# Performance work log

Measured on AMD Instinct MI355X. Metric: run time of the kernel, lower is better.

Reference implementation:

```python
import jax, jax.numpy as jnp
import numpy as np

D_MODEL = 1024
MLP_DIM = 4096
N_EXPERTS = 8
B, T = 4, 1024


def setup_inputs() -> dict:
    key = jax.random.key(0)
    ks = jax.random.split(key, 7)
    scale_in = (1.0 / D_MODEL) ** 0.5
    scale_out = (1.0 / MLP_DIM) ** 0.5
    # router (PyTorch Linear default init approximated with uniform kaiming-like bound)
    bound_g = (1.0 / D_MODEL) ** 0.5
    w_gate = jax.random.uniform(ks[0], (D_MODEL, N_EXPERTS), minval=-bound_g, maxval=bound_g, dtype=jnp.float32)
    b_gate = jax.random.uniform(ks[1], (N_EXPERTS,), minval=-bound_g, maxval=bound_g, dtype=jnp.float32)
    # expert weights per module's _init_weights: uniform(+-scale), zero biases
    W1 = jax.random.uniform(ks[2], (N_EXPERTS, D_MODEL, MLP_DIM), minval=-scale_in, maxval=scale_in, dtype=jnp.float32)
    b1 = jnp.zeros((N_EXPERTS, MLP_DIM), dtype=jnp.float32)
    W2 = jax.random.uniform(ks[3], (N_EXPERTS, MLP_DIM, D_MODEL), minval=-scale_out, maxval=scale_out, dtype=jnp.float32)
    b2 = jnp.zeros((N_EXPERTS, D_MODEL), dtype=jnp.float32)
    x = jax.random.normal(ks[4], (B, T, D_MODEL), dtype=jnp.float32)
    return {"x": x, "w_gate": w_gate, "b_gate": b_gate, "W1": W1, "b1": b1, "W2": W2, "b2": b2}


def reference(x, w_gate, b_gate, W1, b1, W2, b2):
    b, t, d = x.shape
    x_flat = x.reshape(b * t, d)                       # (N, d)
    # --- SwitchGate: top-1 routing (eval mode, no noise) ---
    logits = x_flat @ w_gate + b_gate                  # (N, E)
    probs = jax.nn.softmax(logits, axis=-1)
    route_p = jnp.max(probs, axis=-1)                  # (N,)
    route_idx = jnp.argmax(probs, axis=-1)             # (N,)
    # --- dense dispatch: run every expert on all tokens, select per-token ---
    h = jnp.einsum('nd,edm->enm', x_flat, W1) + b1[:, None, :]   # (E, N, mlp)
    h = jax.nn.relu(h)
    y = jnp.einsum('enm,emd->end', h, W2) + b2[:, None, :]       # (E, N, d)
    n = b * t
    out = y[route_idx, jnp.arange(n)] * route_p[:, None]         # (N, d)
    return out.reshape(b, t, d)
```

## Files before the change

### kernel.cpp

```cpp
#include <hip/hip_runtime.h>
#include <hip/hip_bf16.h>


#define D_MODEL 1024
#define MLP_DIM 4096
#define N_EXPERTS 8
#define N_TOK 4096
#define KSPLIT 4

__global__ __launch_bounds__(64) void router_kernel(
    const float* __restrict__ x, const float* __restrict__ w_gate,
    const float* __restrict__ b_gate, int* __restrict__ route_idx,
    float* __restrict__ route_p) {
  int t = blockIdx.x;
  int lane = threadIdx.x;
  const float* xr = x + (size_t)t * D_MODEL;
  float acc[N_EXPERTS];
#pragma unroll
  for (int e = 0; e < N_EXPERTS; ++e) acc[e] = 0.f;
#pragma unroll
  for (int i = 0; i < D_MODEL / 64; ++i) {
    int idx = i * 64 + lane;
    float xv = xr[idx];
    const float* wg = w_gate + (size_t)idx * N_EXPERTS;
#pragma unroll
    for (int e = 0; e < N_EXPERTS; ++e) acc[e] += xv * wg[e];
  }
#pragma unroll
  for (int off = 32; off >= 1; off >>= 1) {
#pragma unroll
    for (int e = 0; e < N_EXPERTS; ++e) acc[e] += __shfl_xor(acc[e], off, 64);
  }
  if (lane == 0) {
    float l[N_EXPERTS];
#pragma unroll
    for (int e = 0; e < N_EXPERTS; ++e) l[e] = acc[e] + b_gate[e];
    float m = l[0];
    int bi = 0;
#pragma unroll
    for (int e = 1; e < N_EXPERTS; ++e) {
      if (l[e] > m) { m = l[e]; bi = e; }
    }
    float s = 0.f;
#pragma unroll
    for (int e = 0; e < N_EXPERTS; ++e) s += expf(l[e] - m);
    route_idx[t] = bi;
    route_p[t] = 1.0f / s;
  }
}

__global__ void bucket_kernel(const int* __restrict__ route_idx,
                              int* __restrict__ counts,
                              int* __restrict__ bucket) {
  int t = blockIdx.x * blockDim.x + threadIdx.x;
  if (t < N_TOK) {
    int e = route_idx[t];
    int pos = atomicAdd(&counts[e], 1);
    bucket[e * N_TOK + pos] = t;
  }
}

template <bool SPLIT>
__global__ __launch_bounds__(256) void expert_gemm(
    const float* __restrict__ A, const float* __restrict__ B,
    const float* __restrict__ bias, float* __restrict__ C0,
    float* __restrict__ partials, const int* __restrict__ bucket,
    const int* __restrict__ counts, int Kstride, int Ncols) {
  constexpr int BM = 128, BN = 128, BK = 16;
  constexpr int LDA = BM + 4, LDB = BN + 4;
  int e, kbeg, kend;
  float* Cp;
  if (SPLIT) {
    e = blockIdx.y >> 2;
    int s = blockIdx.y & 3;
    kbeg = s * (MLP_DIM / KSPLIT);
    kend = kbeg + (MLP_DIM / KSPLIT);
    Cp = (s == 0) ? C0 : partials + (size_t)(s - 1) * N_TOK * D_MODEL;
  } else {
    e = blockIdx.y;
    kbeg = 0;
    kend = Kstride;
    Cp = C0;
  }
  int cnt = counts[e];
  int row0 = blockIdx.z * BM;
  if (row0 >= cnt) return;
  int col0 = blockIdx.x * BN;

  __shared__ float As[BK][LDA];
  __shared__ float Bs[BK][LDB];
  __shared__ int tokS[BM];

  int tid = threadIdx.x;
  if (tid < BM) {
    int r = row0 + tid;
    tokS[tid] = (r < cnt) ? bucket[e * N_TOK + r] : -1;
  }
  __syncthreads();

  const int ar = tid >> 2;
  const int ak = (tid & 3) * 4;
  const int bk = tid >> 4;
  const int bj = (tid & 15) * 8;

  const int tx = tid & 15;
  const int ty = tid >> 4;

  float acc[2][2][4][4];
#pragma unroll
  for (int hm = 0; hm < 2; ++hm)
#pragma unroll
    for (int hn = 0; hn < 2; ++hn)
#pragma unroll
      for (int i = 0; i < 4; ++i)
#pragma unroll
        for (int j = 0; j < 4; ++j) acc[hm][hn][i][j] = 0.f;

  const int tok0 = tokS[ar], tok1 = tokS[ar + 64];
  const float* __restrict__ Ap0 =
      (tok0 >= 0) ? A + (size_t)tok0 * Kstride + ak : nullptr;
  const float* __restrict__ Ap1 =
      (tok1 >= 0) ? A + (size_t)tok1 * Kstride + ak : nullptr;
  const float* __restrict__ Bp =
      B + (size_t)e * Kstride * Ncols + (size_t)bk * Ncols + col0 + bj;

  float4 a0, a1, b0, b1;
  a0 = make_float4(0.f, 0.f, 0.f, 0.f);
  a1 = a0;
  if (Ap0) a0 = *(const float4*)(Ap0 + kbeg);
  if (Ap1) a1 = *(const float4*)(Ap1 + kbeg);
  {
    const float* bp = Bp + (size_t)kbeg * Ncols;
    b0 = *(const float4*)bp;
    b1 = *(const float4*)(bp + 4);
  }

  for (int k0 = kbeg; k0 < kend; k0 += BK) {
    __syncthreads();
    As[ak + 0][ar] = a0.x; As[ak + 1][ar] = a0.y;
    As[ak + 2][ar] = a0.z; As[ak + 3][ar] = a0.w;
    As[ak + 0][ar + 64] = a1.x; As[ak + 1][ar + 64] = a1.y;
    As[ak + 2][ar + 64] = a1.z; As[ak + 3][ar + 64] = a1.w;
    *(float4*)&Bs[bk][bj] = b0;
    *(float4*)&Bs[bk][bj + 4] = b1;
    __syncthreads();

    if (k0 + BK < kend) {
      int kn = k0 + BK;
      a0 = make_float4(0.f, 0.f, 0.f, 0.f);
      a1 = a0;
      if (Ap0) a0 = *(const float4*)(Ap0 + kn);
      if (Ap1) a1 = *(const float4*)(Ap1 + kn);
      const float* bp = Bp + (size_t)kn * Ncols;
      b0 = *(const float4*)bp;
      b1 = *(const float4*)(bp + 4);
    }

#pragma unroll
    for (int kk = 0; kk < BK; ++kk) {
      float av[2][4], bv[2][4];
      *(float4*)&av[0][0] = *(const float4*)&As[kk][ty * 4];
      *(float4*)&av[1][0] = *(const float4*)&As[kk][ty * 4 + 64];
      *(float4*)&bv[0][0] = *(const float4*)&Bs[kk][tx * 4];
      *(float4*)&bv[1][0] = *(const float4*)&Bs[kk][tx * 4 + 64];
#pragma unroll
      for (int hm = 0; hm < 2; ++hm)
#pragma unroll
        for (int hn = 0; hn < 2; ++hn)
#pragma unroll
          for (int i = 0; i < 4; ++i)
#pragma unroll
            for (int j = 0; j < 4; ++j)
              acc[hm][hn][i][j] += av[hm][i] * bv[hn][j];
    }
  }

  if (SPLIT) {
#pragma unroll
    for (int hm = 0; hm < 2; ++hm) {
#pragma unroll
      for (int i = 0; i < 4; ++i) {
        int r = hm * 64 + ty * 4 + i;
        if (row0 + r < cnt) {
          int tok = tokS[r];
#pragma unroll
          for (int hn = 0; hn < 2; ++hn) {
            float4 o;
            o.x = acc[hm][hn][i][0]; o.y = acc[hm][hn][i][1];
            o.z = acc[hm][hn][i][2]; o.w = acc[hm][hn][i][3];
            *(float4*)(Cp + (size_t)tok * Ncols + col0 + hn * 64 + tx * 4) = o;
          }
        }
      }
    }
  } else {
    float4 bvv[2];
    bvv[0] = *(const float4*)(bias + (size_t)e * Ncols + col0 + tx * 4);
    bvv[1] = *(const float4*)(bias + (size_t)e * Ncols + col0 + tx * 4 + 64);
#pragma unroll
    for (int hm = 0; hm < 2; ++hm) {
#pragma unroll
      for (int i = 0; i < 4; ++i) {
        int r = hm * 64 + ty * 4 + i;
        if (row0 + r < cnt) {
          int tok = tokS[r];
#pragma unroll
          for (int hn = 0; hn < 2; ++hn) {
            const float* bb = (const float*)&bvv[hn];
            float4 o;
            o.x = fmaxf(acc[hm][hn][i][0] + bb[0], 0.f);
            o.y = fmaxf(acc[hm][hn][i][1] + bb[1], 0.f);
            o.z = fmaxf(acc[hm][hn][i][2] + bb[2], 0.f);
            o.w = fmaxf(acc[hm][hn][i][3] + bb[3], 0.f);
            *(float4*)(Cp + (size_t)tok * Ncols + col0 + hn * 64 + tx * 4) = o;
          }
        }
      }
    }
  }
}

__global__ __launch_bounds__(256) void moe_reduce_kernel(
    float* __restrict__ out, const float* __restrict__ partials,
    const float* __restrict__ b2, const int* __restrict__ route_idx,
    const float* __restrict__ route_p) {
  int tok = blockIdx.x;
  int c = threadIdx.x * 4;
  int e = route_idx[tok];
  float p = route_p[tok];
  size_t off = (size_t)tok * D_MODEL + c;
  float4 s = *(const float4*)(out + off);
  const size_t stride = (size_t)N_TOK * D_MODEL;
#pragma unroll
  for (int sp = 0; sp < KSPLIT - 1; ++sp) {
    float4 v = *(const float4*)(partials + sp * stride + off);
    s.x += v.x; s.y += v.y; s.z += v.z; s.w += v.w;
  }
  float4 bv = *(const float4*)(b2 + (size_t)e * D_MODEL + c);
  s.x = (s.x + bv.x) * p;
  s.y = (s.y + bv.y) * p;
  s.z = (s.z + bv.z) * p;
  s.w = (s.w + bv.w) * p;
  *(float4*)(out + off) = s;
}

extern "C" void kernel_launch(void* const* d_in, const int* in_sizes, int n_in,
                              void* d_out, int out_size, void* d_ws,
                              size_t ws_size, hipStream_t stream) {
  const float* x = (const float*)d_in[0];
  const float* w_gate = (const float*)d_in[1];
  const float* b_gate = (const float*)d_in[2];
  const float* W1 = (const float*)d_in[3];
  const float* b1 = (const float*)d_in[4];
  const float* W2 = (const float*)d_in[5];
  const float* b2 = (const float*)d_in[6];
  float* out = (float*)d_out;

  char* ws = (char*)d_ws;
  int* route_idx = (int*)ws;
  float* route_p = (float*)(ws + 16384);
  int* counts = (int*)(ws + 32768);
  int* bucket = (int*)(ws + 33024);
  float* H = (float*)(ws + 164096);
  float* partials = (float*)(ws + 164096 + (size_t)67108864);

  hipMemsetAsync(counts, 0, N_EXPERTS * sizeof(int), stream);
  router_kernel<<<N_TOK, 64, 0, stream>>>(x, w_gate, b_gate, route_idx, route_p);
  bucket_kernel<<<N_TOK / 256, 256, 0, stream>>>(route_idx, counts, bucket);
  expert_gemm<false><<<dim3(MLP_DIM / 128, N_EXPERTS, N_TOK / 128), 256, 0,
                       stream>>>(x, W1, b1, H, nullptr, bucket, counts,
                                 D_MODEL, MLP_DIM);
  expert_gemm<true><<<dim3(D_MODEL / 128, N_EXPERTS * KSPLIT, N_TOK / 128), 256,
                      0, stream>>>(H, W2, nullptr, out, partials, bucket,
                                   counts, MLP_DIM, D_MODEL);
  moe_reduce_kernel<<<N_TOK, 256, 0, stream>>>(out, partials, b2, route_idx,
                                               route_p);
}
```

Before: 1.268 ms.

## Schedule expert GEMMs from compact tile worklist and double-buffer shared memory

Adds a single-thread worklist kernel that lists only the non-empty (expert, row-block) tiles. Both expert GEMMs now launch a flat grid of 1280 blocks that index into that list with an XCD-aware interleaved mapping, instead of a 3D grid where most blocks exit early. The shared-memory A/B tiles are double-buffered so each iteration needs one barrier instead of two. The costs are an extra tiny serial kernel launch and twice the shared memory per block, and the grid caps the worklist at 40 tiles, which holds for 4096 tokens over 8 experts.

```diff
diff --git a/kernel.cpp b/kernel.cpp
--- a/kernel.cpp
+++ b/kernel.cpp
@@ -7,6 +7,9 @@
 #define N_EXPERTS 8
 #define N_TOK 4096
 #define KSPLIT 4
+#define WLMAX 40
+#define NWG 1280
+#define CHUNK (NWG / 8)
 
 __global__ __launch_bounds__(64) void router_kernel(
     const float* __restrict__ x, const float* __restrict__ w_gate,
@@ -60,38 +63,64 @@
   }
 }
 
+__global__ void worklist_kernel(const int* __restrict__ counts,
+                                int* __restrict__ mlist_e,
+                                int* __restrict__ mlist_r,
+                                int* __restrict__ Mp) {
+  if (threadIdx.x == 0) {
+    int m = 0;
+    for (int e = 0; e < N_EXPERTS; ++e) {
+      int c = counts[e];
+      for (int r = 0; r < c; r += 128) {
+        mlist_e[m] = e;
+        mlist_r[m] = r;
+        ++m;
+      }
+    }
+    *Mp = m;
+  }
+}
+
 template <bool SPLIT>
 __global__ __launch_bounds__(256) void expert_gemm(
     const float* __restrict__ A, const float* __restrict__ B,
     const float* __restrict__ bias, float* __restrict__ C0,
     float* __restrict__ partials, const int* __restrict__ bucket,
-    const int* __restrict__ counts, int Kstride, int Ncols) {
+    const int* __restrict__ counts, const int* __restrict__ mlist_e,
+    const int* __restrict__ mlist_r, const int* __restrict__ Mp,
+    int Kstride, int Ncols) {
   constexpr int BM = 128, BN = 128, BK = 16;
   constexpr int LDA = BM + 4, LDB = BN + 4;
-  int e, kbeg, kend;
+  const int L = blockIdx.x;
+  const int w = (L & 7) * CHUNK + (L >> 3);
+  int m, colblk, kbeg, kend;
   float* Cp;
   if (SPLIT) {
-    e = blockIdx.y >> 2;
-    int s = blockIdx.y & 3;
+    m = w % WLMAX;
+    int cs = w / WLMAX;
+    colblk = cs & 7;
+    int s = cs >> 3;
     kbeg = s * (MLP_DIM / KSPLIT);
     kend = kbeg + (MLP_DIM / KSPLIT);
     Cp = (s == 0) ? C0 : partials + (size_t)(s - 1) * N_TOK * D_MODEL;
   } else {
-    e = blockIdx.y;
+    m = w % WLMAX;
+    colblk = w / WLMAX;
     kbeg = 0;
     kend = Kstride;
     Cp = C0;
   }
-  int cnt = counts[e];
-  int row0 = blockIdx.z * BM;
-  if (row0 >= cnt) return;
-  int col0 = blockIdx.x * BN;
-
-  __shared__ float As[BK][LDA];
-  __shared__ float Bs[BK][LDB];
+  if (m >= *Mp) return;
+  const int e = mlist_e[m];
+  const int row0 = mlist_r[m];
+  const int cnt = counts[e];
+  const int col0 = colblk * BN;
+
+  __shared__ float As[2][BK][LDA];
+  __shared__ float Bs[2][BK][LDB];
   __shared__ int tokS[BM];
 
-  int tid = threadIdx.x;
+  const int tid = threadIdx.x;
   if (tid < BM) {
     int r = row0 + tid;
     tokS[tid] = (r < cnt) ? bucket[e * N_TOK + r] : -1;
@@ -125,44 +154,50 @@
       B + (size_t)e * Kstride * Ncols + (size_t)bk * Ncols + col0 + bj;
 
   float4 a0, a1, b0, b1;
-  a0 = make_float4(0.f, 0.f, 0.f, 0.f);
-  a1 = a0;
-  if (Ap0) a0 = *(const float4*)(Ap0 + kbeg);
-  if (Ap1) a1 = *(const float4*)(Ap1 + kbeg);
-  {
-    const float* bp = Bp + (size_t)kbeg * Ncols;
-    b0 = *(const float4*)bp;
-    b1 = *(const float4*)(bp + 4);
-  }
-
-  for (int k0 = kbeg; k0 < kend; k0 += BK) {
-    __syncthreads();
-    As[ak + 0][ar] = a0.x; As[ak + 1][ar] = a0.y;
-    As[ak + 2][ar] = a0.z; As[ak + 3][ar] = a0.w;
-    As[ak + 0][ar + 64] = a1.x; As[ak + 1][ar + 64] = a1.y;
-    As[ak + 2][ar + 64] = a1.z; As[ak + 3][ar + 64] = a1.w;
-    *(float4*)&Bs[bk][bj] = b0;
-    *(float4*)&Bs[bk][bj + 4] = b1;
-    __syncthreads();
-
-    if (k0 + BK < kend) {
-      int kn = k0 + BK;
-      a0 = make_float4(0.f, 0.f, 0.f, 0.f);
-      a1 = a0;
-      if (Ap0) a0 = *(const float4*)(Ap0 + kn);
-      if (Ap1) a1 = *(const float4*)(Ap1 + kn);
-      const float* bp = Bp + (size_t)kn * Ncols;
-      b0 = *(const float4*)bp;
-      b1 = *(const float4*)(bp + 4);
+
+#define LOADTILE(K0)                                          \
+  a0 = make_float4(0.f, 0.f, 0.f, 0.f);                       \
+  a1 = a0;                                                    \
+  if (Ap0) a0 = *(const float4*)(Ap0 + (K0));                 \
+  if (Ap1) a1 = *(const float4*)(Ap1 + (K0));                 \
+  {                                                           \
+    const float* bp = Bp + (size_t)(K0) * Ncols;              \
+    b0 = *(const float4*)bp;                                  \
+    b1 = *(const float4*)(bp + 4);                            \
+  }
+
+#define WRITETILE(BUF)                                        \
+  As[BUF][ak + 0][ar] = a0.x;                                 \
+  As[BUF][ak + 1][ar] = a0.y;                                 \
+  As[BUF][ak + 2][ar] = a0.z;                                 \
+  As[BUF][ak + 3][ar] = a0.w;                                 \
+  As[BUF][ak + 0][ar + 64] = a1.x;                            \
+  As[BUF][ak + 1][ar + 64] = a1.y;                            \
+  As[BUF][ak + 2][ar + 64] = a1.z;                            \
+  As[BUF][ak + 3][ar + 64] = a1.w;                            \
+  *(float4*)&Bs[BUF][bk][bj] = b0;                            \
+  *(float4*)&Bs[BUF][bk][bj + 4] = b1;
+
+  LOADTILE(kbeg);
+  WRITETILE(0);
+  __syncthreads();
+
+  const int nt = (kend - kbeg) / BK;
+  for (int t = 0; t < nt; ++t) {
+    const int cur = t & 1;
+    const bool more = (t + 1 < nt);
+    if (more) {
+      const int kn = kbeg + (t + 1) * BK;
+      LOADTILE(kn);
     }
 
 #pragma unroll
     for (int kk = 0; kk < BK; ++kk) {
       float av[2][4], bv[2][4];
-      *(float4*)&av[0][0] = *(const float4*)&As[kk][ty * 4];
-      *(float4*)&av[1][0] = *(const float4*)&As[kk][ty * 4 + 64];
-      *(float4*)&bv[0][0] = *(const float4*)&Bs[kk][tx * 4];
-      *(float4*)&bv[1][0] = *(const float4*)&Bs[kk][tx * 4 + 64];
+      *(float4*)&av[0][0] = *(const float4*)&As[cur][kk][ty * 4];
+      *(float4*)&av[1][0] = *(const float4*)&As[cur][kk][ty * 4 + 64];
+      *(float4*)&bv[0][0] = *(const float4*)&Bs[cur][kk][tx * 4];
+      *(float4*)&bv[1][0] = *(const float4*)&Bs[cur][kk][tx * 4 + 64];
 #pragma unroll
       for (int hm = 0; hm < 2; ++hm)
 #pragma unroll
@@ -173,7 +208,15 @@
             for (int j = 0; j < 4; ++j)
               acc[hm][hn][i][j] += av[hm][i] * bv[hn][j];
     }
-  }
+
+    if (more) {
+      WRITETILE(cur ^ 1);
+      __syncthreads();
+    }
+  }
+
+#undef LOADTILE
+#undef WRITETILE
 
   if (SPLIT) {
 #pragma unroll
@@ -186,8 +229,10 @@
 #pragma unroll
           for (int hn = 0; hn < 2; ++hn) {
             float4 o;
-            o.x = acc[hm][hn][i][0]; o.y = acc[hm][hn][i][1];
-            o.z = acc[hm][hn][i][2]; o.w = acc[hm][hn][i][3];
+            o.x = acc[hm][hn][i][0];
+            o.y = acc[hm][hn][i][1];
+            o.z = acc[hm][hn][i][2];
+            o.w = acc[hm][hn][i][3];
             *(float4*)(Cp + (size_t)tok * Ncols + col0 + hn * 64 + tx * 4) = o;
           }
         }
@@ -260,19 +305,23 @@
   int* route_idx = (int*)ws;
   float* route_p = (float*)(ws + 16384);
   int* counts = (int*)(ws + 32768);
-  int* bucket = (int*)(ws + 33024);
-  float* H = (float*)(ws + 164096);
-  float* partials = (float*)(ws + 164096 + (size_t)67108864);
+  int* Mp = (int*)(ws + 32896);
+  int* mlist_e = (int*)(ws + 33024);
+  int* mlist_r = (int*)(ws + 33280);
+  int* bucket = (int*)(ws + 33536);
+  float* H = (float*)(ws + 165888);
+  float* partials = (float*)(ws + 165888 + (size_t)67108864);
 
   hipMemsetAsync(counts, 0, N_EXPERTS * sizeof(int), stream);
   router_kernel<<<N_TOK, 64, 0, stream>>>(x, w_gate, b_gate, route_idx, route_p);
   bucket_kernel<<<N_TOK / 256, 256, 0, stream>>>(route_idx, counts, bucket);
-  expert_gemm<false><<<dim3(MLP_DIM / 128, N_EXPERTS, N_TOK / 128), 256, 0,
-                       stream>>>(x, W1, b1, H, nullptr, bucket, counts,
-                                 D_MODEL, MLP_DIM);
-  expert_gemm<true><<<dim3(D_MODEL / 128, N_EXPERTS * KSPLIT, N_TOK / 128), 256,
-                      0, stream>>>(H, W2, nullptr, out, partials, bucket,
-                                   counts, MLP_DIM, D_MODEL);
+  worklist_kernel<<<1, 64, 0, stream>>>(counts, mlist_e, mlist_r, Mp);
+  expert_gemm<false><<<NWG, 256, 0, stream>>>(x, W1, b1, H, nullptr, bucket,
+                                              counts, mlist_e, mlist_r, Mp,
+                                              D_MODEL, MLP_DIM);
+  expert_gemm<true><<<NWG, 256, 0, stream>>>(H, W2, nullptr, out, partials,
+                                             bucket, counts, mlist_e, mlist_r,
+                                             Mp, MLP_DIM, D_MODEL);
   moe_reduce_kernel<<<N_TOK, 256, 0, stream>>>(out, partials, b2, route_idx,
                                                route_p);
 }
```

After: 1.661 ms. +30.9%, slower.
